# Kernel tuning notes

Hardware: AMD Instinct MI355X
Metric: run time of the kernel (lower is better)

Reference implementation:

```python
import jax, jax.numpy as jnp
import numpy as np

V = 32000; D = 1024; L = 2; H = 16; KVH = 4; HD = D // H; E = 8; FF = 2048; K = 2
B = 2; S = 1024; WINDOW = 4096; THETA = 10000.0; EPS = 1e-6


def setup_inputs() -> dict:
    key = jax.random.key(0)
    ks = jax.random.split(key, 12)
    std = 0.02
    return {
        'tokens': jax.random.randint(ks[0], (B, S), 0, V),
        'tok_emb': jax.random.normal(ks[1], (V, D), jnp.float32),  # nn.Embedding default N(0,1)
        'norm1_w': jnp.ones((L, D), jnp.float32),
        'norm2_w': jnp.ones((L, D), jnp.float32),
        'wq': jax.random.normal(ks[2], (L, D, D), jnp.float32) * std,
        'wk': jax.random.normal(ks[3], (L, KVH * HD, D), jnp.float32) * std,
        'wv': jax.random.normal(ks[4], (L, KVH * HD, D), jnp.float32) * std,
        'wo': jax.random.normal(ks[5], (L, D, D), jnp.float32) * std,
        'router_w': jax.random.normal(ks[6], (L, E, D), jnp.float32) * (std / np.sqrt(D)),
        'w1': jax.random.normal(ks[7], (L, E, FF, D), jnp.float32) * std,
        'w2': jax.random.normal(ks[8], (L, E, FF, D), jnp.float32) * std,
        'w3': jax.random.normal(ks[9], (L, E, D, FF), jnp.float32) * std,
        'normf_w': jnp.ones((D,), jnp.float32),
        'head_w': jax.random.normal(ks[10], (V, D), jnp.float32) * std,
    }


def rmsnorm(x, w):
    # F.normalize(x, dim=-1, eps) * w * sqrt(d)
    n = jnp.linalg.norm(x, axis=-1, keepdims=True)
    return x / jnp.maximum(n, EPS) * w * np.float32(np.sqrt(x.shape[-1]))


def rope(x, cos, sin):
    # x: (b, s, h, hd); pairs are interleaved (even, odd) per view_as_complex
    x2 = x.reshape(x.shape[:-1] + (-1, 2))
    x0, x1 = x2[..., 0], x2[..., 1]
    o0 = x0 * cos - x1 * sin
    o1 = x0 * sin + x1 * cos
    return jnp.stack([o0, o1], axis=-1).reshape(x.shape)


def attention(x, wq, wk, wv, wo, cos, sin):
    b, s, _ = x.shape
    q = (x @ wq.T).reshape(b, s, H, HD)
    k = (x @ wk.T).reshape(b, s, KVH, HD)
    v = (x @ wv.T).reshape(b, s, KVH, HD)
    q = rope(q, cos, sin)
    k = rope(k, cos, sin)
    g = H // KVH
    k = jnp.repeat(k, g, axis=2)
    v = jnp.repeat(v, g, axis=2)
    scores = jnp.einsum('bqhd,bkhd->bhqk', q, k) / np.float32(np.sqrt(HD))
    i = jnp.arange(s)[:, None]; j = jnp.arange(s)[None, :]
    allow = (j <= i) & (i - j < WINDOW)  # causal + sliding window
    scores = jnp.where(allow, scores, -jnp.inf)
    attn = jax.nn.softmax(scores, axis=-1)
    out = jnp.einsum('bhqk,bkhd->bqhd', attn, v).reshape(b, s, D)
    return out @ wo.T


def moe(x, router_w, w1, w2, w3):
    b, s, d = x.shape
    logits = jnp.einsum('bsd,ed->bse', x, router_w)
    probs = jax.nn.softmax(logits, axis=-1)
    _, idx = jax.lax.top_k(probs, K)                      # (b, s, K)
    mask = jax.nn.one_hot(idx, E, dtype=x.dtype).sum(-2)  # (b, s, E) binary
    xt = x.reshape(-1, d)           # (T, d)
    mt = mask.reshape(-1, E)        # (T, E)
    # Dense masked dispatch: every expert computed on all tokens, combine masks to zero
    u = jnp.einsum('td,efd->etf', xt, w1)
    g = jax.nn.silu(u) * jnp.einsum('td,efd->etf', xt, w2)
    y = jnp.einsum('etf,edf->etd', g, w3)
    out = jnp.einsum('etd,te->td', y, mt).reshape(b, s, d)  # unweighted combine (per source)
    # aux losses
    z_loss = jnp.mean(jax.scipy.special.logsumexp(logits, axis=-1)) ** 2
    load = probs.sum(axis=0)  # (s, E), matching probs.sum(dim=0) in source
    load_loss = (jnp.std(load, ddof=1) / jnp.mean(load)) ** 2
    aux = 0.001 * z_loss + 0.001 * load_loss
    return out, aux


def _rope_tables(dtype):
    freqs = 1.0 / (THETA ** (np.arange(0, HD, 2, dtype=np.float32) / HD))
    ang = np.arange(S, dtype=np.float32)[:, None] * freqs[None, :]
    cos = jnp.asarray(np.cos(ang), dtype)[None, :, None, :]
    sin = jnp.asarray(np.sin(ang), dtype)[None, :, None, :]
    return cos, sin


def reference(tokens, tok_emb, norm1_w, norm2_w, wq, wk, wv, wo, router_w, w1, w2, w3, normf_w, head_w):
    x = tok_emb[tokens]  # (B, S, D)
    cos, sin = _rope_tables(x.dtype)
    attn_scale = np.float32(1.0 / np.sqrt(2.0 * L))
    aux_total = jnp.zeros((), x.dtype)
    for l in range(L):
        x = x + attn_scale * attention(rmsnorm(x, norm1_w[l]), wq[l], wk[l], wv[l], wo[l], cos, sin)
        mo, aux = moe(rmsnorm(x, norm2_w[l]), router_w[l], w1[l], w2[l], w3[l])
        x = x + mo
        aux_total = aux_total + aux
    logits = rmsnorm(x, normf_w) @ head_w.T
    return logits, aux_total
```

## Files before the change

### kernel.cpp

```cpp
#include <hip/hip_runtime.h>
#include <math.h>

#define DEV __device__ __forceinline__

using v8s = __attribute__((ext_vector_type(8))) short;
using v4f = __attribute__((ext_vector_type(4))) float;

DEV short f2bf(float f) {
    unsigned u = __float_as_uint(f);
    unsigned r = (u + 0x7fffu + ((u >> 16) & 1u)) >> 16;
    return (short)(unsigned short)r;
}
DEV float bf2f(short s) {
    return __uint_as_float(((unsigned)(unsigned short)s) << 16);
}
DEV unsigned pack2(short a, short b) {
    return ((unsigned)(unsigned short)a) | (((unsigned)(unsigned short)b) << 16);
}

DEV float block_sum256(float v, float* red) {
    __syncthreads();
#pragma unroll
    for (int o = 32; o >= 1; o >>= 1) v += __shfl_down(v, o, 64);
    if ((threadIdx.x & 63) == 0) red[threadIdx.x >> 6] = v;
    __syncthreads();
    return red[0] + red[1] + red[2] + red[3];
}
DEV float block_max256(float v, float* red) {
    __syncthreads();
#pragma unroll
    for (int o = 32; o >= 1; o >>= 1) v = fmaxf(v, __shfl_down(v, o, 64));
    if ((threadIdx.x & 63) == 0) red[threadIdx.x >> 6] = v;
    __syncthreads();
    return fmaxf(fmaxf(red[0], red[1]), fmaxf(red[2], red[3]));
}


struct GemmP {
    const short* Ah; const short* Al;
    const float* B;
    float* C; short* Ch; short* Cl;
    const int* cnt; const int* prefix; const int* ltok; const int* lrow;
    long strideAz, strideBz, strideCz;
    int M, N, K, lda, ldb, ldc;
    float alpha;
    int outMode;
    int gqaB;
    int attnC;
    int grouped;
    int causalSkip;
    int causalK;
};

template<bool SPLIT>
__global__ __launch_bounds__(256) void gemm_bt(GemmP p) {
    const int tid = threadIdx.x;
    const int z = blockIdx.z, mt = blockIdx.y, nt = blockIdx.x;
    if (p.causalSkip && nt > mt) return;

    int Mz = p.M;
    const int* ltokz = nullptr; const int* lrowz = nullptr; int pz = 0;
    if (p.grouped) {
        Mz = p.cnt[z]; pz = p.prefix[z];
        ltokz = p.ltok + z * 2048; lrowz = p.lrow + z * 2048;
    }
    if (mt * 128 >= Mz) return;

    long aOff = (long)z * p.strideAz;
    long bOff, cOff;
    if (p.gqaB) { int b = z >> 4, h = z & 15; bOff = (long)(b * 4 + (h >> 2)) * p.strideBz; }
    else bOff = (long)z * p.strideBz;
    if (p.attnC) { int b = z >> 4, h = z & 15; cOff = (long)b * 1048576 + h * 64; }
    else cOff = (long)z * p.strideCz;

    extern __shared__ char smem[];
    short* Ahs = (short*)smem;
    short* Bhs = Ahs + 4096;
    short* Als = Bhs + 4096;
    short* Bls = Als + 4096;

    const int lane = tid & 63, w = tid >> 6;
    const int lr = lane & 15, lg = lane >> 4;
    const int wr = w >> 1, wc = w & 1;

    v4f acc[4][4];
#pragma unroll
    for (int i = 0; i < 4; ++i)
#pragma unroll
        for (int j = 0; j < 4; ++j) { acc[i][j][0] = 0.f; acc[i][j][1] = 0.f; acc[i][j][2] = 0.f; acc[i][j][3] = 0.f; }

    const int srow = tid >> 1;
    const int sseg = tid & 1;

    int am = mt * 128 + srow; if (am >= Mz) am = Mz - 1;
    long arowoff;
    if (p.grouped == 1)      arowoff = (long)ltokz[am] * p.lda;
    else if (p.grouped == 2) arowoff = (long)(pz + am) * p.lda;
    else                     arowoff = aOff + (long)am * p.lda;
    int bn = nt * 128 + srow; if (bn >= p.N) bn = p.N - 1;
    long browoff = bOff + (long)bn * p.ldb;

    const int kEnd = p.causalK ? min(p.K, (mt + 1) * 128) : p.K;

    for (int k0 = 0; k0 < kEnd; k0 += 32) {
        __syncthreads();
        const int kb = k0 + sseg * 16;
        const int kg = sseg * 2;
        {
            const uint4* src = (const uint4*)(p.Ah + arowoff + kb);
            uint4 h0 = src[0], h1 = src[1];
            *(uint4*)(Ahs + (kg * 128 + srow) * 8) = h0;
            *(uint4*)(Ahs + ((kg + 1) * 128 + srow) * 8) = h1;
            if (SPLIT) {
                const uint4* sl = (const uint4*)(p.Al + arowoff + kb);
                uint4 l0 = sl[0], l1 = sl[1];
                *(uint4*)(Als + (kg * 128 + srow) * 8) = l0;
                *(uint4*)(Als + ((kg + 1) * 128 + srow) * 8) = l1;
            }
        }
        {
            const float* bp = p.B + browoff + kb;
#pragma unroll
            for (int q = 0; q < 2; ++q) {
                float4 fa = *(const float4*)(bp + q * 8);
                float4 fb = *(const float4*)(bp + q * 8 + 4);
                short h0 = f2bf(fa.x), h1 = f2bf(fa.y), h2 = f2bf(fa.z), h3 = f2bf(fa.w);
                short h4 = f2bf(fb.x), h5 = f2bf(fb.y), h6 = f2bf(fb.z), h7 = f2bf(fb.w);
                uint4 hp = make_uint4(pack2(h0, h1), pack2(h2, h3), pack2(h4, h5), pack2(h6, h7));
                *(uint4*)(Bhs + ((kg + q) * 128 + srow) * 8) = hp;
                if (SPLIT) {
                    short l0 = f2bf(fa.x - bf2f(h0)), l1 = f2bf(fa.y - bf2f(h1));
                    short l2 = f2bf(fa.z - bf2f(h2)), l3 = f2bf(fa.w - bf2f(h3));
                    short l4 = f2bf(fb.x - bf2f(h4)), l5 = f2bf(fb.y - bf2f(h5));
                    short l6 = f2bf(fb.z - bf2f(h6)), l7 = f2bf(fb.w - bf2f(h7));
                    uint4 lp = make_uint4(pack2(l0, l1), pack2(l2, l3), pack2(l4, l5), pack2(l6, l7));
                    *(uint4*)(Bls + ((kg + q) * 128 + srow) * 8) = lp;
                }
            }
        }
        __syncthreads();
        const int abase = lg * 128 * 8 + (wr * 64 + lr) * 8;
        const int bbase = lg * 128 * 8 + (wc * 64 + lr) * 8;
        v8s ah[4], bh[4];
#pragma unroll
        for (int i = 0; i < 4; ++i) {
            ah[i] = *(const v8s*)(Ahs + abase + i * 16 * 8);
            bh[i] = *(const v8s*)(Bhs + bbase + i * 16 * 8);
        }
        if constexpr (SPLIT) {
            v8s al[4], bl[4];
#pragma unroll
            for (int i = 0; i < 4; ++i) {
                al[i] = *(const v8s*)(Als + abase + i * 16 * 8);
                bl[i] = *(const v8s*)(Bls + bbase + i * 16 * 8);
            }
#pragma unroll
            for (int mi = 0; mi < 4; ++mi)
#pragma unroll
                for (int nj = 0; nj < 4; ++nj) {
                    acc[mi][nj] = __builtin_amdgcn_mfma_f32_16x16x32_bf16(ah[mi], bh[nj], acc[mi][nj], 0, 0, 0);
                    acc[mi][nj] = __builtin_amdgcn_mfma_f32_16x16x32_bf16(al[mi], bh[nj], acc[mi][nj], 0, 0, 0);
                    acc[mi][nj] = __builtin_amdgcn_mfma_f32_16x16x32_bf16(ah[mi], bl[nj], acc[mi][nj], 0, 0, 0);
                }
        } else {
#pragma unroll
            for (int mi = 0; mi < 4; ++mi)
#pragma unroll
                for (int nj = 0; nj < 4; ++nj)
                    acc[mi][nj] = __builtin_amdgcn_mfma_f32_16x16x32_bf16(ah[mi], bh[nj], acc[mi][nj], 0, 0, 0);
        }
    }

#pragma unroll
    for (int mi = 0; mi < 4; ++mi) {
        const int mrow = mt * 128 + wr * 64 + mi * 16 + lg * 4;
#pragma unroll
        for (int nj = 0; nj < 4; ++nj) {
            const int ncol = nt * 128 + wc * 64 + nj * 16 + lr;
            if (ncol < p.N) {
#pragma unroll
                for (int r = 0; r < 4; ++r) {
                    const int m = mrow + r;
                    if (m < Mz) {
                        float v = acc[mi][nj][r] * p.alpha;
                        long crow;
                        if (p.grouped == 1) crow = pz + m;
                        else if (p.grouped == 2) crow = lrowz[m];
                        else crow = m;
                        long co = cOff + crow * (long)p.ldc + ncol;
                        if (p.outMode == 0) p.C[co] = v;
                        else if (p.outMode == 1) p.C[co] += v;
                        else {
                            short hi = f2bf(v);
                            p.Ch[co] = hi;
                            p.Cl[co] = f2bf(v - bf2f(hi));
                        }
                    }
                }
            }
        }
    }
}

__global__ __launch_bounds__(256) void embed_kernel(const int* toks, const float* emb, float* X) {
    const int t = blockIdx.x;
    const int tok = toks[t];
    const float4* s = (const float4*)(emb + (size_t)tok * 1024);
    float4* d = (float4*)(X + (size_t)t * 1024);
    d[threadIdx.x] = s[threadIdx.x];
}

__global__ __launch_bounds__(256) void rmsnorm_split(const float* X, const float* w, short* oh, short* ol) {
    __shared__ float red[4];
    const long t = blockIdx.x;
    const float* r = X + t * 1024;
    float ss = 0.f;
    for (int j = threadIdx.x; j < 1024; j += 256) { float f = r[j]; ss += f * f; }
    ss = block_sum256(ss, red);
    const float sc = 32.f / fmaxf(sqrtf(ss), 1e-6f);
    for (int j = threadIdx.x; j < 1024; j += 256) {
        float f = r[j] * sc * w[j];
        short hi = f2bf(f);
        oh[t * 1024 + j] = hi;
        ol[t * 1024 + j] = f2bf(f - bf2f(hi));
    }
}

struct RopeF { float f[32]; };

__global__ __launch_bounds__(256) void rope_q_kernel(const float* Q, short* OH, short* OL, RopeF rf) {
    const int idx = blockIdx.x * 256 + threadIdx.x;
    const int pp = idx & 31, h = (idx >> 5) & 15, s = (idx >> 9) & 1023, b = idx >> 19;
    const float* src = Q + ((size_t)(b * 1024 + s)) * 1024 + h * 64 + 2 * pp;
    const float x0 = src[0], x1 = src[1];
    const float ang = (float)s * rf.f[pp];
    float sn, cs; sincosf(ang, &sn, &cs);
    const float o0 = x0 * cs - x1 * sn, o1 = x0 * sn + x1 * cs;
    const size_t o = ((size_t)((b * 16 + h) * 1024 + s)) * 64 + 2 * pp;
    short h0 = f2bf(o0); OH[o] = h0; OL[o] = f2bf(o0 - bf2f(h0));
    short h1 = f2bf(o1); OH[o + 1] = h1; OL[o + 1] = f2bf(o1 - bf2f(h1));
}

__global__ __launch_bounds__(256) void rope_k_kernel(const float* Kin, float* KR, RopeF rf) {
    const int idx = blockIdx.x * 256 + threadIdx.x;
    const int pp = idx & 31, kv = (idx >> 5) & 3, s = (idx >> 7) & 1023, b = idx >> 17;
    const float* src = Kin + ((size_t)(b * 1024 + s)) * 256 + kv * 64 + 2 * pp;
    const float x0 = src[0], x1 = src[1];
    const float ang = (float)s * rf.f[pp];
    float sn, cs; sincosf(ang, &sn, &cs);
    const size_t o = ((size_t)((b * 4 + kv) * 1024 + s)) * 64 + 2 * pp;
    KR[o] = x0 * cs - x1 * sn;
    KR[o + 1] = x0 * sn + x1 * cs;
}

__global__ __launch_bounds__(256) void transpose_v_kernel(const float* Vin, float* VT) {
    const int idx = blockIdx.x * 256 + threadIdx.x;
    const int d = idx & 63, kv = (idx >> 6) & 3, s = (idx >> 8) & 1023, b = idx >> 18;
    VT[((size_t)((b * 4 + kv) * 64 + d)) * 1024 + s] = Vin[idx];
}

__global__ __launch_bounds__(256) void attn_softmax(float* SC) {
    const long row = blockIdx.x;
    const int i = (int)(row & 1023);
    float* r = SC + row * 1024;
    __shared__ float buf[1024];
    __shared__ float red[4];
    const int n = i + 1;
    for (int j = threadIdx.x; j < 1024; j += 256) buf[j] = r[j];
    __syncthreads();
    float m = -INFINITY;
    for (int j = threadIdx.x; j < n; j += 256) m = fmaxf(m, buf[j]);
    m = block_max256(m, red);
    float s = 0.f;
    for (int j = threadIdx.x; j < n; j += 256) { float e = expf(buf[j] - m); buf[j] = e; s += e; }
    s = block_sum256(s, red);
    const float inv = 1.f / s;
    short* rh = (short*)r;
    short* rl = rh + 1024;
    __syncthreads();
    for (int j = threadIdx.x; j < 1024; j += 256) {
        float pv = (j < n) ? buf[j] * inv : 0.f;
        short hi = f2bf(pv);
        rh[j] = hi;
        rl[j] = f2bf(pv - bf2f(hi));
    }
}

__global__ __launch_bounds__(256) void router_kernel(const float* X, const float* wn, const float* rw,
                                                     float* probs, float* lse, int* cnt, int* ltok, int* lrow) {
    __shared__ float xs[1024];
    __shared__ float red[4];
    __shared__ float lg[8];
    const int t = blockIdx.x;
    const float* r = X + (size_t)t * 1024;
    for (int j = threadIdx.x; j < 1024; j += 256) xs[j] = r[j];
    __syncthreads();
    float ss = 0.f;
    for (int j = threadIdx.x; j < 1024; j += 256) ss += xs[j] * xs[j];
    ss = block_sum256(ss, red);
    const float sc = 32.f / fmaxf(sqrtf(ss), 1e-6f);
    float acc[8] = {0, 0, 0, 0, 0, 0, 0, 0};
    for (int j = threadIdx.x; j < 1024; j += 256) {
        const float xv = xs[j] * wn[j];
#pragma unroll
        for (int e = 0; e < 8; ++e) acc[e] += xv * rw[e * 1024 + j];
    }
#pragma unroll
    for (int e = 0; e < 8; ++e) {
        float s = block_sum256(acc[e], red);
        if (threadIdx.x == 0) lg[e] = s * sc;
    }
    __syncthreads();
    if (threadIdx.x == 0) {
        float m = lg[0];
        for (int e = 1; e < 8; ++e) m = fmaxf(m, lg[e]);
        float ex[8], se = 0.f;
        for (int e = 0; e < 8; ++e) { ex[e] = expf(lg[e] - m); se += ex[e]; }
        const float inv = 1.f / se;
        float pr[8];
        for (int e = 0; e < 8; ++e) { pr[e] = ex[e] * inv; probs[(size_t)t * 8 + e] = pr[e]; }
        lse[t] = m + logf(se);
        int i1 = 0;
        for (int e = 1; e < 8; ++e) if (pr[e] > pr[i1]) i1 = e;
        int i2 = (i1 == 0) ? 1 : 0;
        for (int e = 0; e < 8; ++e) if (e != i1 && pr[e] > pr[i2]) i2 = e;
        int s1 = atomicAdd(&cnt[i1], 1); ltok[i1 * 2048 + s1] = t; lrow[i1 * 2048 + s1] = 2 * t;
        int s2 = atomicAdd(&cnt[i2], 1); ltok[i2 * 2048 + s2] = t; lrow[i2 * 2048 + s2] = 2 * t + 1;
    }
}

__global__ void prefix_kernel(const int* cnt, int* pref) {
    if (threadIdx.x == 0 && blockIdx.x == 0) {
        int a = 0;
        for (int e = 0; e < 8; ++e) { pref[e] = a; a += cnt[e]; }
    }
}

__global__ __launch_bounds__(256) void silu_mul(const float* U, const float* G, short* HH, short* HL) {
    const long idx = (long)blockIdx.x * 256 + threadIdx.x;
    const float u = U[idx], g = G[idx];
    const float h = (u / (1.f + expf(-u))) * g;
    short hi = f2bf(h);
    HH[idx] = hi;
    HL[idx] = f2bf(h - bf2f(hi));
}

__global__ __launch_bounds__(256) void combine_kernel(float* X, const float* Y) {
    const int idx = blockIdx.x * 256 + threadIdx.x;
    const int t = idx >> 10, d = idx & 1023;
    X[idx] += Y[((size_t)(2 * t)) * 1024 + d] + Y[((size_t)(2 * t + 1)) * 1024 + d];
}

__global__ __launch_bounds__(256) void aux_kernel(const float* probs, const float* lse, float* auxb, int layer) {
    __shared__ float red[4];
    float sl = 0.f;
    for (int t = threadIdx.x; t < 2048; t += 256) sl += lse[t];
    sl = block_sum256(sl, red);
    float s1 = 0.f, s2 = 0.f;
    for (int i = threadIdx.x; i < 8192; i += 256) {
        const float l = probs[i] + probs[8192 + i];
        s1 += l; s2 += l * l;
    }
    s1 = block_sum256(s1, red);
    s2 = block_sum256(s2, red);
    if (threadIdx.x == 0) {
        const float ml = sl / 2048.f;
        const float mean = s1 / 8192.f;
        const float var = fmaxf((s2 - s1 * s1 / 8192.f) / 8191.f, 0.f);
        auxb[layer] = 0.001f * (ml * ml + var / (mean * mean));
    }
}

__global__ void finalize_aux(const float* auxb, float* out) {
    if (threadIdx.x == 0 && blockIdx.x == 0)
        out[(size_t)2 * 1024 * 32000] = auxb[0] + auxb[1];
}

static void run_gemm(hipStream_t s, bool split, const GemmP& p, int gx, int gy, int gz) {
    dim3 g(gx, gy, gz), b(256);
    if (split) gemm_bt<true><<<g, b, 32768, s>>>(p);
    else       gemm_bt<false><<<g, b, 16384, s>>>(p);
}

extern "C" void kernel_launch(void* const* d_in, const int* in_sizes, int n_in,
                              void* d_out, int out_size, void* d_ws, size_t ws_size,
                              hipStream_t stream) {
    (void)in_sizes; (void)n_in; (void)out_size; (void)ws_size;
    const int*   tokens = (const int*)d_in[0];
    const float* tok_emb = (const float*)d_in[1];
    const float* norm1 = (const float*)d_in[2];
    const float* norm2 = (const float*)d_in[3];
    const float* wq = (const float*)d_in[4];
    const float* wk = (const float*)d_in[5];
    const float* wv = (const float*)d_in[6];
    const float* wo = (const float*)d_in[7];
    const float* rw = (const float*)d_in[8];
    const float* w1 = (const float*)d_in[9];
    const float* w2 = (const float*)d_in[10];
    const float* w3 = (const float*)d_in[11];
    const float* normf = (const float*)d_in[12];
    const float* headw = (const float*)d_in[13];
    float* out = (float*)d_out;

    char* w = (char*)d_ws;
    const size_t MB = 1024ull * 1024ull;
    float* X    = (float*)(w + 0);
    short* XNH  = (short*)(w + 8 * MB);
    short* XNL  = (short*)(w + 12 * MB);
    short* QRH  = (short*)(w + 16 * MB);
    short* QRL  = (short*)(w + 20 * MB);
    float* KR   = (float*)(w + 24 * MB);
    float* VT   = (float*)(w + 26 * MB);
    short* AOH  = (short*)(w + 28 * MB);
    short* AOL  = (short*)(w + 32 * MB);
    float* SC   = (float*)(w + 36 * MB);
    float* U    = (float*)(w + 164 * MB);
    float* G    = (float*)(w + 196 * MB);
    short* HH   = (short*)(w + 228 * MB);
    short* HL   = (short*)(w + 244 * MB);
    float* PROBS= (float*)(w + 260 * MB);
    float* LSE  = (float*)(w + 260 * MB + 65536);
    int*   CNT  = (int*)  (w + 260 * MB + 73728);
    int*   PREF = (int*)  (w + 260 * MB + 73856);
    int*   LTOK = (int*)  (w + 260 * MB + 74240);
    int*   LROW = (int*)  (w + 260 * MB + 74240 + 65536);
    float* AUXB = (float*)(w + 260 * MB + 74240 + 131072);

    float* QTMP = SC;
    float* KTMP = SC + 2097152;
    float* VTMP = SC + 2621440;

    RopeF rf;
    for (int i = 0; i < 32; ++i) {
        float t = (float)pow(10000.0, (double)(2 * i) / 64.0);
        rf.f[i] = 1.0f / t;
    }

    embed_kernel<<<2048, 256, 0, stream>>>(tokens, tok_emb, X);

    for (int l = 0; l < 2; ++l) {
        rmsnorm_split<<<2048, 256, 0, stream>>>(X, norm1 + l * 1024, XNH, XNL);

        { GemmP p = {}; p.Ah = XNH; p.Al = XNL; p.B = wq + (size_t)l * 1024 * 1024; p.C = QTMP;
          p.M = 2048; p.N = 1024; p.K = 1024; p.lda = 1024; p.ldb = 1024; p.ldc = 1024; p.alpha = 1.f;
          run_gemm(stream, true, p, 8, 16, 1); }
        { GemmP p = {}; p.Ah = XNH; p.Al = XNL; p.B = wk + (size_t)l * 256 * 1024; p.C = KTMP;
          p.M = 2048; p.N = 256; p.K = 1024; p.lda = 1024; p.ldb = 1024; p.ldc = 256; p.alpha = 1.f;
          run_gemm(stream, true, p, 2, 16, 1); }
        { GemmP p = {}; p.Ah = XNH; p.Al = XNL; p.B = wv + (size_t)l * 256 * 1024; p.C = VTMP;
          p.M = 2048; p.N = 256; p.K = 1024; p.lda = 1024; p.ldb = 1024; p.ldc = 256; p.alpha = 1.f;
          run_gemm(stream, true, p, 2, 16, 1); }

        rope_q_kernel<<<4096, 256, 0, stream>>>(QTMP, QRH, QRL, rf);
        rope_k_kernel<<<1024, 256, 0, stream>>>(KTMP, KR, rf);
        transpose_v_kernel<<<2048, 256, 0, stream>>>(VTMP, VT);

        { GemmP p = {}; p.Ah = QRH; p.Al = QRL; p.B = KR; p.C = SC;
          p.M = 1024; p.N = 1024; p.K = 64; p.lda = 64; p.ldb = 64; p.ldc = 1024;
          p.strideAz = 65536; p.strideBz = 65536; p.strideCz = 1048576;
          p.alpha = 0.125f; p.gqaB = 1; p.causalSkip = 1;
          run_gemm(stream, true, p, 8, 8, 32); }

        attn_softmax<<<32768, 256, 0, stream>>>(SC);

        { GemmP p = {}; p.Ah = (short*)SC; p.Al = (short*)SC + 1024; p.B = VT; p.Ch = AOH; p.Cl = AOL;
          p.M = 1024; p.N = 64; p.K = 1024; p.lda = 2048; p.ldb = 1024; p.ldc = 1024;
          p.strideAz = 2097152; p.strideBz = 65536;
          p.alpha = 1.f; p.gqaB = 1; p.attnC = 1; p.causalK = 1; p.outMode = 2;
          run_gemm(stream, true, p, 1, 8, 32); }

        { GemmP p = {}; p.Ah = AOH; p.Al = AOL; p.B = wo + (size_t)l * 1024 * 1024; p.C = X;
          p.M = 2048; p.N = 1024; p.K = 1024; p.lda = 1024; p.ldb = 1024; p.ldc = 1024;
          p.alpha = 0.5f; p.outMode = 1;
          run_gemm(stream, true, p, 8, 16, 1); }

        rmsnorm_split<<<2048, 256, 0, stream>>>(X, norm2 + l * 1024, XNH, XNL);
        hipMemsetAsync(CNT, 0, 8 * sizeof(int), stream);
        router_kernel<<<2048, 256, 0, stream>>>(X, norm2 + l * 1024, rw + (size_t)l * 8 * 1024,
                                                PROBS, LSE, CNT, LTOK, LROW);
        prefix_kernel<<<1, 64, 0, stream>>>(CNT, PREF);

        const bool msp = (l == 0);
        { GemmP p = {}; p.Ah = XNH; p.Al = XNL; p.B = w1 + (size_t)l * 8 * 2048 * 1024; p.C = U;
          p.M = 2048; p.N = 2048; p.K = 1024; p.lda = 1024; p.ldb = 1024; p.ldc = 2048;
          p.strideBz = 2097152; p.alpha = 1.f; p.grouped = 1;
          p.cnt = CNT; p.prefix = PREF; p.ltok = LTOK; p.lrow = LROW;
          run_gemm(stream, msp, p, 16, 16, 8); }
        { GemmP p = {}; p.Ah = XNH; p.Al = XNL; p.B = w2 + (size_t)l * 8 * 2048 * 1024; p.C = G;
          p.M = 2048; p.N = 2048; p.K = 1024; p.lda = 1024; p.ldb = 1024; p.ldc = 2048;
          p.strideBz = 2097152; p.alpha = 1.f; p.grouped = 1;
          p.cnt = CNT; p.prefix = PREF; p.ltok = LTOK; p.lrow = LROW;
          run_gemm(stream, msp, p, 16, 16, 8); }
        silu_mul<<<32768, 256, 0, stream>>>(U, G, HH, HL);
        { GemmP p = {}; p.Ah = HH; p.Al = HL; p.B = w3 + (size_t)l * 8 * 1024 * 2048; p.C = U;
          p.M = 2048; p.N = 1024; p.K = 2048; p.lda = 2048; p.ldb = 2048; p.ldc = 1024;
          p.strideBz = 2097152; p.alpha = 1.f; p.grouped = 2;
          p.cnt = CNT; p.prefix = PREF; p.ltok = LTOK; p.lrow = LROW;
          run_gemm(stream, msp, p, 8, 16, 8); }
        combine_kernel<<<8192, 256, 0, stream>>>(X, U);
        aux_kernel<<<1, 256, 0, stream>>>(PROBS, LSE, AUXB, l);
    }

    rmsnorm_split<<<2048, 256, 0, stream>>>(X, normf, XNH, XNL);
    { GemmP p = {}; p.Ah = XNH; p.B = headw; p.C = out;
      p.M = 2048; p.N = 32000; p.K = 1024; p.lda = 1024; p.ldb = 1024; p.ldc = 32000; p.alpha = 1.f;
      run_gemm(stream, false, p, 250, 16, 1); }
    finalize_aux<<<1, 1, 0, stream>>>(AUXB, out);
}
```

Baseline: 2.273 ms.

## Pre-convert weights to bf16 hi/lo, fuse QKV and W1/W2 GEMMs, remap tiles per XCD

Adds a conversion kernel that turns fp32 weights into bf16 hi/lo planes once per call, so the GEMM loads bf16 directly instead of converting fp32 B tiles inside every K-loop iteration. Fuses the Q/K/V projections into one N=1536 GEMM and interleaves W1/W2 into one N=4096 grouped GEMM, then reads the gate from the same buffer in a vectorised silu_mul. Replaces the 3D grid with a 1D launch that keeps M-tiles of the same column group on one XCD for L2 reuse, and vectorises the combine kernel. The extra conversion passes over all weights, including the large head and expert matrices, add memory traffic on every call.

```diff
diff --git a/kernel.cpp b/kernel.cpp
--- a/kernel.cpp
+++ b/kernel.cpp
@@ -14,9 +14,6 @@
 DEV float bf2f(short s) {
     return __uint_as_float(((unsigned)(unsigned short)s) << 16);
 }
-DEV unsigned pack2(short a, short b) {
-    return ((unsigned)(unsigned short)a) | (((unsigned)(unsigned short)b) << 16);
-}
 
 DEV float block_sum256(float v, float* red) {
     __syncthreads();
@@ -36,9 +33,28 @@
 }
 
 
+__global__ __launch_bounds__(256) void conv_kernel(const float* __restrict__ src,
+                                                   short* __restrict__ hi, short* __restrict__ lo,
+                                                   long total4, long chunk4, long dstStride4) {
+    for (long i = (long)blockIdx.x * 256 + threadIdx.x; i < total4; i += (long)gridDim.x * 256) {
+        long c = i / chunk4, r = i - c * chunk4;
+        long d = c * dstStride4 + r;
+        float4 f = ((const float4*)src)[i];
+        short h0 = f2bf(f.x), h1 = f2bf(f.y), h2 = f2bf(f.z), h3 = f2bf(f.w);
+        ((ushort4*)hi)[d] = make_ushort4((unsigned short)h0, (unsigned short)h1,
+                                         (unsigned short)h2, (unsigned short)h3);
+        if (lo) {
+            short l0 = f2bf(f.x - bf2f(h0)), l1 = f2bf(f.y - bf2f(h1));
+            short l2 = f2bf(f.z - bf2f(h2)), l3 = f2bf(f.w - bf2f(h3));
+            ((ushort4*)lo)[d] = make_ushort4((unsigned short)l0, (unsigned short)l1,
+                                             (unsigned short)l2, (unsigned short)l3);
+        }
+    }
+}
+
 struct GemmP {
     const short* Ah; const short* Al;
-    const float* B;
+    const short* Bh; const short* Bl;
     float* C; short* Ch; short* Cl;
     const int* cnt; const int* prefix; const int* ltok; const int* lrow;
     long strideAz, strideBz, strideCz;
@@ -50,13 +66,21 @@
     int grouped;
     int causalSkip;
     int causalK;
+    int ntiles, S, G;
 };
 
 template<bool SPLIT>
 __global__ __launch_bounds__(256) void gemm_bt(GemmP p) {
+    const int lid = blockIdx.x;
+    const int xcd = lid & 7, sI = lid >> 3;
+    const int gi = xcd + 8 * (sI / p.S);
+    if (gi >= p.G) return;
+    const int mt = sI % p.S;
+    const int nt = gi % p.ntiles;
+    const int z  = gi / p.ntiles;
+    if (p.causalSkip && nt > mt) return;
+
     const int tid = threadIdx.x;
-    const int z = blockIdx.z, mt = blockIdx.y, nt = blockIdx.x;
-    if (p.causalSkip && nt > mt) return;
 
     int Mz = p.M;
     const int* ltokz = nullptr; const int* lrowz = nullptr; int pz = 0;
@@ -91,6 +115,7 @@
 
     const int srow = tid >> 1;
     const int sseg = tid & 1;
+    const int kg = sseg * 2;
 
     int am = mt * 128 + srow; if (am >= Mz) am = Mz - 1;
     long arowoff;
@@ -98,61 +123,46 @@
     else if (p.grouped == 2) arowoff = (long)(pz + am) * p.lda;
     else                     arowoff = aOff + (long)am * p.lda;
     int bn = nt * 128 + srow; if (bn >= p.N) bn = p.N - 1;
-    long browoff = bOff + (long)bn * p.ldb;
+    const long browoff = bOff + (long)bn * p.ldb;
+
+    const short* aH = p.Ah + arowoff + sseg * 16;
+    const short* bH = p.Bh + browoff + sseg * 16;
+    const short* aL = SPLIT ? p.Al + arowoff + sseg * 16 : nullptr;
+    const short* bL = SPLIT ? p.Bl + browoff + sseg * 16 : nullptr;
+    short* dA0 = Ahs + (kg * 128 + srow) * 8; short* dA1 = dA0 + 1024;
+    short* dB0 = Bhs + (kg * 128 + srow) * 8; short* dB1 = dB0 + 1024;
+    short* dA0l = Als + (kg * 128 + srow) * 8; short* dA1l = dA0l + 1024;
+    short* dB0l = Bls + (kg * 128 + srow) * 8; short* dB1l = dB0l + 1024;
 
     const int kEnd = p.causalK ? min(p.K, (mt + 1) * 128) : p.K;
 
     for (int k0 = 0; k0 < kEnd; k0 += 32) {
         __syncthreads();
-        const int kb = k0 + sseg * 16;
-        const int kg = sseg * 2;
-        {
-            const uint4* src = (const uint4*)(p.Ah + arowoff + kb);
-            uint4 h0 = src[0], h1 = src[1];
-            *(uint4*)(Ahs + (kg * 128 + srow) * 8) = h0;
-            *(uint4*)(Ahs + ((kg + 1) * 128 + srow) * 8) = h1;
-            if (SPLIT) {
-                const uint4* sl = (const uint4*)(p.Al + arowoff + kb);
-                uint4 l0 = sl[0], l1 = sl[1];
-                *(uint4*)(Als + (kg * 128 + srow) * 8) = l0;
-                *(uint4*)(Als + ((kg + 1) * 128 + srow) * 8) = l1;
-            }
-        }
-        {
-            const float* bp = p.B + browoff + kb;
-#pragma unroll
-            for (int q = 0; q < 2; ++q) {
-                float4 fa = *(const float4*)(bp + q * 8);
-                float4 fb = *(const float4*)(bp + q * 8 + 4);
-                short h0 = f2bf(fa.x), h1 = f2bf(fa.y), h2 = f2bf(fa.z), h3 = f2bf(fa.w);
-                short h4 = f2bf(fb.x), h5 = f2bf(fb.y), h6 = f2bf(fb.z), h7 = f2bf(fb.w);
-                uint4 hp = make_uint4(pack2(h0, h1), pack2(h2, h3), pack2(h4, h5), pack2(h6, h7));
-                *(uint4*)(Bhs + ((kg + q) * 128 + srow) * 8) = hp;
-                if (SPLIT) {
-                    short l0 = f2bf(fa.x - bf2f(h0)), l1 = f2bf(fa.y - bf2f(h1));
-                    short l2 = f2bf(fa.z - bf2f(h2)), l3 = f2bf(fa.w - bf2f(h3));
-                    short l4 = f2bf(fb.x - bf2f(h4)), l5 = f2bf(fb.y - bf2f(h5));
-                    short l6 = f2bf(fb.z - bf2f(h6)), l7 = f2bf(fb.w - bf2f(h7));
-                    uint4 lp = make_uint4(pack2(l0, l1), pack2(l2, l3), pack2(l4, l5), pack2(l6, l7));
-                    *(uint4*)(Bls + ((kg + q) * 128 + srow) * 8) = lp;
-                }
-            }
+        *(uint4*)dA0 = *(const uint4*)(aH + k0);
+        *(uint4*)dA1 = *(const uint4*)(aH + k0 + 8);
+        *(uint4*)dB0 = *(const uint4*)(bH + k0);
+        *(uint4*)dB1 = *(const uint4*)(bH + k0 + 8);
+        if (SPLIT) {
+            *(uint4*)dA0l = *(const uint4*)(aL + k0);
+            *(uint4*)dA1l = *(const uint4*)(aL + k0 + 8);
+            *(uint4*)dB0l = *(const uint4*)(bL + k0);
+            *(uint4*)dB1l = *(const uint4*)(bL + k0 + 8);
         }
         __syncthreads();
-        const int abase = lg * 128 * 8 + (wr * 64 + lr) * 8;
-        const int bbase = lg * 128 * 8 + (wc * 64 + lr) * 8;
+        const int abase = lg * 1024 + (wr * 64 + lr) * 8;
+        const int bbase = lg * 1024 + (wc * 64 + lr) * 8;
         v8s ah[4], bh[4];
 #pragma unroll
         for (int i = 0; i < 4; ++i) {
-            ah[i] = *(const v8s*)(Ahs + abase + i * 16 * 8);
-            bh[i] = *(const v8s*)(Bhs + bbase + i * 16 * 8);
+            ah[i] = *(const v8s*)(Ahs + abase + i * 128);
+            bh[i] = *(const v8s*)(Bhs + bbase + i * 128);
         }
         if constexpr (SPLIT) {
             v8s al[4], bl[4];
 #pragma unroll
             for (int i = 0; i < 4; ++i) {
-                al[i] = *(const v8s*)(Als + abase + i * 16 * 8);
-                bl[i] = *(const v8s*)(Bls + bbase + i * 16 * 8);
+                al[i] = *(const v8s*)(Als + abase + i * 128);
+                bl[i] = *(const v8s*)(Bls + bbase + i * 128);
             }
 #pragma unroll
             for (int mi = 0; mi < 4; ++mi)
@@ -228,10 +238,10 @@
 
 struct RopeF { float f[32]; };
 
-__global__ __launch_bounds__(256) void rope_q_kernel(const float* Q, short* OH, short* OL, RopeF rf) {
+__global__ __launch_bounds__(256) void rope_q_kernel(const float* QKV, short* OH, short* OL, RopeF rf) {
     const int idx = blockIdx.x * 256 + threadIdx.x;
     const int pp = idx & 31, h = (idx >> 5) & 15, s = (idx >> 9) & 1023, b = idx >> 19;
-    const float* src = Q + ((size_t)(b * 1024 + s)) * 1024 + h * 64 + 2 * pp;
+    const float* src = QKV + ((size_t)(b * 1024 + s)) * 1536 + h * 64 + 2 * pp;
     const float x0 = src[0], x1 = src[1];
     const float ang = (float)s * rf.f[pp];
     float sn, cs; sincosf(ang, &sn, &cs);
@@ -241,22 +251,26 @@
     short h1 = f2bf(o1); OH[o + 1] = h1; OL[o + 1] = f2bf(o1 - bf2f(h1));
 }
 
-__global__ __launch_bounds__(256) void rope_k_kernel(const float* Kin, float* KR, RopeF rf) {
+__global__ __launch_bounds__(256) void rope_k_kernel(const float* QKV, short* KH, short* KL, RopeF rf) {
     const int idx = blockIdx.x * 256 + threadIdx.x;
     const int pp = idx & 31, kv = (idx >> 5) & 3, s = (idx >> 7) & 1023, b = idx >> 17;
-    const float* src = Kin + ((size_t)(b * 1024 + s)) * 256 + kv * 64 + 2 * pp;
+    const float* src = QKV + ((size_t)(b * 1024 + s)) * 1536 + 1024 + kv * 64 + 2 * pp;
     const float x0 = src[0], x1 = src[1];
     const float ang = (float)s * rf.f[pp];
     float sn, cs; sincosf(ang, &sn, &cs);
+    const float o0 = x0 * cs - x1 * sn, o1 = x0 * sn + x1 * cs;
     const size_t o = ((size_t)((b * 4 + kv) * 1024 + s)) * 64 + 2 * pp;
-    KR[o] = x0 * cs - x1 * sn;
-    KR[o + 1] = x0 * sn + x1 * cs;
-}
-
-__global__ __launch_bounds__(256) void transpose_v_kernel(const float* Vin, float* VT) {
+    short h0 = f2bf(o0); KH[o] = h0; KL[o] = f2bf(o0 - bf2f(h0));
+    short h1 = f2bf(o1); KH[o + 1] = h1; KL[o + 1] = f2bf(o1 - bf2f(h1));
+}
+
+__global__ __launch_bounds__(256) void transpose_v_kernel(const float* QKV, short* VH, short* VL) {
     const int idx = blockIdx.x * 256 + threadIdx.x;
     const int d = idx & 63, kv = (idx >> 6) & 3, s = (idx >> 8) & 1023, b = idx >> 18;
-    VT[((size_t)((b * 4 + kv) * 64 + d)) * 1024 + s] = Vin[idx];
+    const float f = QKV[((size_t)(b * 1024 + s)) * 1536 + 1280 + kv * 64 + d];
+    const size_t o = ((size_t)((b * 4 + kv) * 64 + d)) * 1024 + s;
+    short hi = f2bf(f);
+    VH[o] = hi; VL[o] = f2bf(f - bf2f(hi));
 }
 
 __global__ __launch_bounds__(256) void attn_softmax(float* SC) {
@@ -336,19 +350,34 @@
     }
 }
 
-__global__ __launch_bounds__(256) void silu_mul(const float* U, const float* G, short* HH, short* HL) {
-    const long idx = (long)blockIdx.x * 256 + threadIdx.x;
-    const float u = U[idx], g = G[idx];
-    const float h = (u / (1.f + expf(-u))) * g;
-    short hi = f2bf(h);
-    HH[idx] = hi;
-    HL[idx] = f2bf(h - bf2f(hi));
+__global__ __launch_bounds__(256) void silu_mul(const float* U, short* HH, short* HL) {
+    const long i4 = (long)blockIdx.x * 256 + threadIdx.x;
+    const int f4 = (int)(i4 & 511), row = (int)(i4 >> 9);
+    const float4 u = *(const float4*)(U + ((long)row << 12) + (f4 << 2));
+    const float4 g = *(const float4*)(U + ((long)row << 12) + 2048 + (f4 << 2));
+    float h[4];
+    h[0] = (u.x / (1.f + expf(-u.x))) * g.x;
+    h[1] = (u.y / (1.f + expf(-u.y))) * g.y;
+    h[2] = (u.z / (1.f + expf(-u.z))) * g.z;
+    h[3] = (u.w / (1.f + expf(-u.w))) * g.w;
+    const long o = (long)row * 2048 + (f4 << 2);
+    short h0 = f2bf(h[0]), h1 = f2bf(h[1]), h2 = f2bf(h[2]), h3 = f2bf(h[3]);
+    *(ushort4*)(HH + o) = make_ushort4((unsigned short)h0, (unsigned short)h1,
+                                       (unsigned short)h2, (unsigned short)h3);
+    short l0 = f2bf(h[0] - bf2f(h0)), l1 = f2bf(h[1] - bf2f(h1));
+    short l2 = f2bf(h[2] - bf2f(h2)), l3 = f2bf(h[3] - bf2f(h3));
+    *(ushort4*)(HL + o) = make_ushort4((unsigned short)l0, (unsigned short)l1,
+                                       (unsigned short)l2, (unsigned short)l3);
 }
 
 __global__ __launch_bounds__(256) void combine_kernel(float* X, const float* Y) {
-    const int idx = blockIdx.x * 256 + threadIdx.x;
-    const int t = idx >> 10, d = idx & 1023;
-    X[idx] += Y[((size_t)(2 * t)) * 1024 + d] + Y[((size_t)(2 * t + 1)) * 1024 + d];
+    const int i4 = blockIdx.x * 256 + threadIdx.x;
+    const int t = i4 >> 8, d4 = i4 & 255;
+    float4 x = ((float4*)X)[i4];
+    const float4 a = ((const float4*)Y)[(size_t)(2 * t) * 256 + d4];
+    const float4 b = ((const float4*)Y)[(size_t)(2 * t + 1) * 256 + d4];
+    x.x += a.x + b.x; x.y += a.y + b.y; x.z += a.z + b.z; x.w += a.w + b.w;
+    ((float4*)X)[i4] = x;
 }
 
 __global__ __launch_bounds__(256) void aux_kernel(const float* probs, const float* lse, float* auxb, int layer) {
@@ -376,10 +405,21 @@
         out[(size_t)2 * 1024 * 32000] = auxb[0] + auxb[1];
 }
 
-static void run_gemm(hipStream_t s, bool split, const GemmP& p, int gx, int gy, int gz) {
-    dim3 g(gx, gy, gz), b(256);
+static void run_gemm(hipStream_t s, bool split, GemmP& p, int ntiles, int mtiles, int zdim) {
+    p.ntiles = ntiles; p.S = mtiles;
+    p.G = ntiles * zdim;
+    int Gp = (p.G + 7) & ~7;
+    long nb = (long)Gp * mtiles;
+    dim3 g((unsigned)nb, 1, 1), b(256);
     if (split) gemm_bt<true><<<g, b, 32768, s>>>(p);
     else       gemm_bt<false><<<g, b, 16384, s>>>(p);
+}
+
+static void run_conv(hipStream_t s, const float* src, short* hi, short* lo,
+                     long total, long chunk, long dstStride) {
+    long t4 = total / 4;
+    long nb = (t4 + 255) / 256; if (nb > 2048) nb = 2048;
+    conv_kernel<<<(unsigned)nb, 256, 0, s>>>(src, hi, lo, t4, chunk / 4, dstStride / 4);
 }
 
 extern "C" void kernel_launch(void* const* d_in, const int* in_sizes, int n_in,
@@ -407,28 +447,36 @@
     float* X    = (float*)(w + 0);
     short* XNH  = (short*)(w + 8 * MB);
     short* XNL  = (short*)(w + 12 * MB);
-    short* QRH  = (short*)(w + 16 * MB);
-    short* QRL  = (short*)(w + 20 * MB);
-    float* KR   = (float*)(w + 24 * MB);
-    float* VT   = (float*)(w + 26 * MB);
-    short* AOH  = (short*)(w + 28 * MB);
-    short* AOL  = (short*)(w + 32 * MB);
+    short* AOH  = (short*)(w + 16 * MB);
+    short* AOL  = (short*)(w + 20 * MB);
+    short* QRH  = (short*)(w + 24 * MB);
+    short* QRL  = (short*)(w + 28 * MB);
+    short* KRH  = (short*)(w + 32 * MB);
+    short* KRL  = (short*)(w + 33 * MB);
+    short* VTH  = (short*)(w + 34 * MB);
+    short* VTL  = (short*)(w + 35 * MB);
+    float* QKV  = (float*)(w + 36 * MB);
     float* SC   = (float*)(w + 36 * MB);
-    float* U    = (float*)(w + 164 * MB);
-    float* G    = (float*)(w + 196 * MB);
-    short* HH   = (short*)(w + 228 * MB);
-    short* HL   = (short*)(w + 244 * MB);
-    float* PROBS= (float*)(w + 260 * MB);
-    float* LSE  = (float*)(w + 260 * MB + 65536);
-    int*   CNT  = (int*)  (w + 260 * MB + 73728);
-    int*   PREF = (int*)  (w + 260 * MB + 73856);
-    int*   LTOK = (int*)  (w + 260 * MB + 74240);
-    int*   LROW = (int*)  (w + 260 * MB + 74240 + 65536);
-    float* AUXB = (float*)(w + 260 * MB + 74240 + 131072);
-
-    float* QTMP = SC;
-    float* KTMP = SC + 2097152;
-    float* VTMP = SC + 2621440;
+    float* U    = (float*)(w + 36 * MB);
+    short* HH   = (short*)(w + 100 * MB);
+    short* HL   = (short*)(w + 116 * MB);
+    float* Y    = (float*)(w + 132 * MB);
+    float* PROBS= (float*)(w + 164 * MB);
+    float* LSE  = (float*)(w + 164 * MB + 65536);
+    int*   CNT  = (int*)  (w + 164 * MB + 73728);
+    int*   PREF = (int*)  (w + 164 * MB + 73856);
+    int*   LTOK = (int*)  (w + 164 * MB + 74240);
+    int*   LROW = (int*)  (w + 164 * MB + 74240 + 65536);
+    float* AUXB = (float*)(w + 164 * MB + 74240 + 131072);
+    short* WQKVH = (short*)(w + 166 * MB);
+    short* WQKVL = (short*)(w + 172 * MB);
+    short* WOH   = (short*)(w + 178 * MB);
+    short* WOL   = (short*)(w + 182 * MB);
+    short* W12H  = (short*)(w + 186 * MB);
+    short* W12L  = (short*)(w + 250 * MB);
+    short* W3H   = (short*)(w + 314 * MB);
+    short* W3L   = (short*)(w + 346 * MB);
+    short* HDH   = (short*)(w + 378 * MB);
 
     RopeF rf;
     for (int i = 0; i < 32; ++i) {
@@ -436,26 +484,34 @@
         rf.f[i] = 1.0f / t;
     }
 
+    for (int l = 0; l < 2; ++l) {
+        long qo = (long)l * 1572864;
+        run_conv(stream, wq + (long)l * 1048576, WQKVH + qo,           WQKVL + qo,           1048576, 1048576, 1048576);
+        run_conv(stream, wk + (long)l * 262144,  WQKVH + qo + 1048576, WQKVL + qo + 1048576, 262144,  262144,  262144);
+        run_conv(stream, wv + (long)l * 262144,  WQKVH + qo + 1310720, WQKVL + qo + 1310720, 262144,  262144,  262144);
+    }
+    run_conv(stream, wo, WOH, WOL, 2097152, 2097152, 2097152);
+    run_conv(stream, headw, HDH, nullptr, 32768000, 32768000, 32768000);
+
     embed_kernel<<<2048, 256, 0, stream>>>(tokens, tok_emb, X);
 
     for (int l = 0; l < 2; ++l) {
+        const bool msp = (l == 0);
+        run_conv(stream, w1 + (long)l * 16777216, W12H,           msp ? W12L : nullptr,           16777216, 2097152, 4194304);
+        run_conv(stream, w2 + (long)l * 16777216, W12H + 2097152, msp ? W12L + 2097152 : nullptr, 16777216, 2097152, 4194304);
+        run_conv(stream, w3 + (long)l * 16777216, W3H,            msp ? W3L : nullptr,            16777216, 16777216, 16777216);
+
         rmsnorm_split<<<2048, 256, 0, stream>>>(X, norm1 + l * 1024, XNH, XNL);
 
-        { GemmP p = {}; p.Ah = XNH; p.Al = XNL; p.B = wq + (size_t)l * 1024 * 1024; p.C = QTMP;
-          p.M = 2048; p.N = 1024; p.K = 1024; p.lda = 1024; p.ldb = 1024; p.ldc = 1024; p.alpha = 1.f;
-          run_gemm(stream, true, p, 8, 16, 1); }
-        { GemmP p = {}; p.Ah = XNH; p.Al = XNL; p.B = wk + (size_t)l * 256 * 1024; p.C = KTMP;
-          p.M = 2048; p.N = 256; p.K = 1024; p.lda = 1024; p.ldb = 1024; p.ldc = 256; p.alpha = 1.f;
-          run_gemm(stream, true, p, 2, 16, 1); }
-        { GemmP p = {}; p.Ah = XNH; p.Al = XNL; p.B = wv + (size_t)l * 256 * 1024; p.C = VTMP;
-          p.M = 2048; p.N = 256; p.K = 1024; p.lda = 1024; p.ldb = 1024; p.ldc = 256; p.alpha = 1.f;
-          run_gemm(stream, true, p, 2, 16, 1); }
-
-        rope_q_kernel<<<4096, 256, 0, stream>>>(QTMP, QRH, QRL, rf);
-        rope_k_kernel<<<1024, 256, 0, stream>>>(KTMP, KR, rf);
-        transpose_v_kernel<<<2048, 256, 0, stream>>>(VTMP, VT);
-
-        { GemmP p = {}; p.Ah = QRH; p.Al = QRL; p.B = KR; p.C = SC;
+        { GemmP p = {}; p.Ah = XNH; p.Al = XNL; p.Bh = WQKVH + (long)l * 1572864; p.Bl = WQKVL + (long)l * 1572864;
+          p.C = QKV; p.M = 2048; p.N = 1536; p.K = 1024; p.lda = 1024; p.ldb = 1024; p.ldc = 1536; p.alpha = 1.f;
+          run_gemm(stream, true, p, 12, 16, 1); }
+
+        rope_q_kernel<<<4096, 256, 0, stream>>>(QKV, QRH, QRL, rf);
+        rope_k_kernel<<<1024, 256, 0, stream>>>(QKV, KRH, KRL, rf);
+        transpose_v_kernel<<<2048, 256, 0, stream>>>(QKV, VTH, VTL);
+
+        { GemmP p = {}; p.Ah = QRH; p.Al = QRL; p.Bh = KRH; p.Bl = KRL; p.C = SC;
           p.M = 1024; p.N = 1024; p.K = 64; p.lda = 64; p.ldb = 64; p.ldc = 1024;
           p.strideAz = 65536; p.strideBz = 65536; p.strideCz = 1048576;
           p.alpha = 0.125f; p.gqaB = 1; p.causalSkip = 1;
@@ -463,13 +519,13 @@
 
         attn_softmax<<<32768, 256, 0, stream>>>(SC);
 
-        { GemmP p = {}; p.Ah = (short*)SC; p.Al = (short*)SC + 1024; p.B = VT; p.Ch = AOH; p.Cl = AOL;
+        { GemmP p = {}; p.Ah = (short*)SC; p.Al = (short*)SC + 1024; p.Bh = VTH; p.Bl = VTL; p.Ch = AOH; p.Cl = AOL;
           p.M = 1024; p.N = 64; p.K = 1024; p.lda = 2048; p.ldb = 1024; p.ldc = 1024;
           p.strideAz = 2097152; p.strideBz = 65536;
           p.alpha = 1.f; p.gqaB = 1; p.attnC = 1; p.causalK = 1; p.outMode = 2;
           run_gemm(stream, true, p, 1, 8, 32); }
 
-        { GemmP p = {}; p.Ah = AOH; p.Al = AOL; p.B = wo + (size_t)l * 1024 * 1024; p.C = X;
+        { GemmP p = {}; p.Ah = AOH; p.Al = AOL; p.Bh = WOH + (long)l * 1048576; p.Bl = WOL + (long)l * 1048576; p.C = X;
           p.M = 2048; p.N = 1024; p.K = 1024; p.lda = 1024; p.ldb = 1024; p.ldc = 1024;
           p.alpha = 0.5f; p.outMode = 1;
           run_gemm(stream, true, p, 8, 16, 1); }
@@ -480,29 +536,23 @@
                                                 PROBS, LSE, CNT, LTOK, LROW);
         prefix_kernel<<<1, 64, 0, stream>>>(CNT, PREF);
 
-        const bool msp = (l == 0);
-        { GemmP p = {}; p.Ah = XNH; p.Al = XNL; p.B = w1 + (size_t)l * 8 * 2048 * 1024; p.C = U;
-          p.M = 2048; p.N = 2048; p.K = 1024; p.lda = 1024; p.ldb = 1024; p.ldc = 2048;
-          p.strideBz = 2097152; p.alpha = 1.f; p.grouped = 1;
+        { GemmP p = {}; p.Ah = XNH; p.Al = XNL; p.Bh = W12H; p.Bl = W12L; p.C = U;
+          p.M = 2048; p.N = 4096; p.K = 1024; p.lda = 1024; p.ldb = 1024; p.ldc = 4096;
+          p.strideBz = 4194304; p.alpha = 1.f; p.grouped = 1;
           p.cnt = CNT; p.prefix = PREF; p.ltok = LTOK; p.lrow = LROW;
-          run_gemm(stream, msp, p, 16, 16, 8); }
-        { GemmP p = {}; p.Ah = XNH; p.Al = XNL; p.B = w2 + (size_t)l * 8 * 2048 * 1024; p.C = G;
-          p.M = 2048; p.N = 2048; p.K = 1024; p.lda = 1024; p.ldb = 1024; p.ldc = 2048;
-          p.strideBz = 2097152; p.alpha = 1.f; p.grouped = 1;
-          p.cnt = CNT; p.prefix = PREF; p.ltok = LTOK; p.lrow = LROW;
-          run_gemm(stream, msp, p, 16, 16, 8); }
-        silu_mul<<<32768, 256, 0, stream>>>(U, G, HH, HL);
-        { GemmP p = {}; p.Ah = HH; p.Al = HL; p.B = w3 + (size_t)l * 8 * 1024 * 2048; p.C = U;
+          run_gemm(stream, msp, p, 32, 16, 8); }
+        silu_mul<<<8192, 256, 0, stream>>>(U, HH, HL);
+        { GemmP p = {}; p.Ah = HH; p.Al = HL; p.Bh = W3H; p.Bl = W3L; p.C = Y;
           p.M = 2048; p.N = 1024; p.K = 2048; p.lda = 2048; p.ldb = 2048; p.ldc = 1024;
           p.strideBz = 2097152; p.alpha = 1.f; p.grouped = 2;
           p.cnt = CNT; p.prefix = PREF; p.ltok = LTOK; p.lrow = LROW;
           run_gemm(stream, msp, p, 8, 16, 8); }
-        combine_kernel<<<8192, 256, 0, stream>>>(X, U);
+        combine_kernel<<<2048, 256, 0, stream>>>(X, Y);
         aux_kernel<<<1, 256, 0, stream>>>(PROBS, LSE, AUXB, l);
     }
 
     rmsnorm_split<<<2048, 256, 0, stream>>>(X, normf, XNH, XNL);
-    { GemmP p = {}; p.Ah = XNH; p.B = headw; p.C = out;
+    { GemmP p = {}; p.Ah = XNH; p.Bh = HDH; p.C = out;
       p.M = 2048; p.N = 32000; p.K = 1024; p.lda = 1024; p.ldb = 1024; p.ldc = 32000; p.alpha = 1.f;
       run_gemm(stream, false, p, 250, 16, 1); }
     finalize_aux<<<1, 1, 0, stream>>>(AUXB, out);
```

New measurement: 1.930 ms. 1.18x faster.
